# Kernel tuning notes

Hardware: AMD Instinct MI355X
Metric: run time of the kernel (lower is better)

Reference implementation:

```python
import jax, jax.numpy as jnp
import numpy as np

N_SRC = 100000
E = 300000
D = 256
HEADS = 8
D_K = D // HEADS
N_EXPERTS = 5


def setup_inputs() -> dict:
    key = jax.random.key(0)
    kx, ki, ke, kw, kb = jax.random.split(key, 5)
    x = jax.random.normal(kx, (N_SRC, D), dtype=jnp.float32)
    index = jax.random.randint(ki, (E,), 0, N_SRC)
    # disjoint routing masks: each output row handled by exactly one of 5 linears
    expert_id = jax.random.randint(ke, (E,), 0, N_EXPERTS)
    masks = expert_id[None, :] == jnp.arange(N_EXPERTS)[:, None]  # [5, E] bool
    # learned params: 5 independent Linear(D, D) layers (torch layout: y = x @ W.T + b)
    bound = 1.0 / np.sqrt(D)
    W = jax.random.uniform(kw, (N_EXPERTS, D, D), minval=-bound, maxval=bound, dtype=jnp.float32)
    b = jax.random.uniform(kb, (N_EXPERTS, D), minval=-bound, maxval=bound, dtype=jnp.float32)
    return {"x": x, "W": W, "b": b, "index": index, "masks": masks}


def reference(x, W, b, index, masks):
    # gather source rows for every output slot: [E, D]
    xi = x[index]
    out = jnp.zeros((xi.shape[0], D), dtype=x.dtype)
    # sequential masked overwrite matches torch's output[mask] = ... semantics
    for i in range(N_EXPERTS):
        yi = xi @ W[i].T + b[i]  # [E, D]
        out = jnp.where(masks[i][:, None], yi, out)
    return out.reshape(xi.shape[0], HEADS, D_K)
```

## Files before the change

kernel.cpp:

```cpp
#include <hip/hip_runtime.h>

#define E_TOT   300000
#define D_DIM   256
#define N_EXP   5
#define BM      64
#define LDK     264
#define LDF     260
#define NB_CNT  ((E_TOT + 255) / 256)
#define MAX_TILES (E_TOT / BM + N_EXP)

typedef __attribute__((ext_vector_type(8))) short bf16x8;
typedef __attribute__((ext_vector_type(4))) float f32x4;

__device__ inline unsigned short f2bf(float f) {
  union { float f; unsigned u; } v; v.f = f;
  unsigned u = v.u;
  u += 0x7FFFu + ((u >> 16) & 1u);
  return (unsigned short)(u >> 16);
}

__device__ inline int get_expert(const void* masks, int e, bool is_u8) {
  if (is_u8) {
    const unsigned char* m = (const unsigned char*)masks;
#pragma unroll
    for (int i = 0; i < N_EXP; ++i) if (m[(size_t)i * E_TOT + e]) return i;
  } else {
    const int* m = (const int*)masks;
#pragma unroll
    for (int i = 0; i < N_EXP; ++i) if (m[(size_t)i * E_TOT + e]) return i;
  }
  return 0;
}

__global__ void scatter_conv_kernel(const float* __restrict__ W,
                                    unsigned short* __restrict__ Wbf,
                                    const void* __restrict__ masks,
                                    int* __restrict__ cursor, int* __restrict__ perm,
                                    int doConv) {
  __shared__ int wc[4][N_EXP];
  __shared__ int wo[4][N_EXP];
  __shared__ int bb[N_EXP];
  __shared__ int s_u8ok;
  const int tt = threadIdx.x, w = tt >> 6, lane = tt & 63;
  const int e = (int)blockIdx.x * 256 + tt;

  const unsigned char* m8 = (const unsigned char*)masks;
  int cnt1 = 1, ex = -1;
  if (e < E_TOT) {
    cnt1 = 0; int exu = 0;
#pragma unroll
    for (int i = 0; i < N_EXP; ++i) {
      int tb = (m8[(size_t)i * E_TOT + e] != 0);
      cnt1 += tb; if (tb) exu = i;
    }
    ex = exu;
  }
  if (tt == 0) s_u8ok = 1;
  __syncthreads();
  if (cnt1 != 1) s_u8ok = 0;
  __syncthreads();
  if (!s_u8ok && e < E_TOT) ex = get_expert(masks, e, false);

  unsigned long long myBal = 0;
#pragma unroll
  for (int i = 0; i < N_EXP; ++i) {
    unsigned long long bal = __ballot(ex == i);
    if (lane == 0) wc[w][i] = __popcll(bal);
    if (ex == i) myBal = bal;
  }
  if (doConv) {
    const int n4 = (N_EXP * D_DIM * D_DIM) / 4;
    for (int i = e; i < n4; i += (int)gridDim.x * 256) {
      float4 v = ((const float4*)W)[i];
      ushort4 o4;
      o4.x = f2bf(v.x); o4.y = f2bf(v.y); o4.z = f2bf(v.z); o4.w = f2bf(v.w);
      ((ushort4*)Wbf)[i] = o4;
    }
  }
  __syncthreads();
  if (tt < 4 * N_EXP) {
    int ww = tt / N_EXP, ii = tt % N_EXP;
    int s = 0;
    for (int p = 0; p < ww; ++p) s += wc[p][ii];
    wo[ww][ii] = s;
  }
  if (tt < N_EXP) {
    int tot = wc[0][tt] + wc[1][tt] + wc[2][tt] + wc[3][tt];
    int old = atomicAdd(&cursor[tt], tot);
    bb[tt] = tt * E_TOT + old;
  }
  __syncthreads();
  if (ex >= 0) {
    int rank = __popcll(myBal & ((1ull << lane) - 1ull));
    perm[bb[ex] + wo[w][ex] + rank] = e;
  }
}

__global__ void prep_kernel(const float* __restrict__ W, unsigned short* __restrict__ Wbf,
                            const void* __restrict__ masks, int* __restrict__ hdr,
                            int doConv) {
  __shared__ int wc[4][N_EXP];
  __shared__ int s_u8ok;
  const int tt = threadIdx.x, w = tt >> 6, lane = tt & 63;
  const int gtid = (int)blockIdx.x * 256 + tt;

  const unsigned char* m8 = (const unsigned char*)masks;
  int cnt1 = 1, ex = -1;
  if (gtid < E_TOT) {
    cnt1 = 0; int exu = 0;
#pragma unroll
    for (int i = 0; i < N_EXP; ++i) {
      int tb = (m8[(size_t)i * E_TOT + gtid] != 0);
      cnt1 += tb; if (tb) exu = i;
    }
    ex = exu;
  }
  if (tt == 0) s_u8ok = 1;
  __syncthreads();
  if (cnt1 != 1) s_u8ok = 0;
  __syncthreads();
  const int is_u8 = s_u8ok;
  if (!is_u8 && gtid < E_TOT) ex = get_expert(masks, gtid, false);

#pragma unroll
  for (int i = 0; i < N_EXP; ++i) {
    unsigned long long bal = __ballot(ex == i);
    if (lane == 0) wc[w][i] = __popcll(bal);
  }
  if (doConv) {
    const int n4 = (N_EXP * D_DIM * D_DIM) / 4;
    for (int i = gtid; i < n4; i += (int)gridDim.x * 256) {
      float4 v = ((const float4*)W)[i];
      ushort4 o4;
      o4.x = f2bf(v.x); o4.y = f2bf(v.y); o4.z = f2bf(v.z); o4.w = f2bf(v.w);
      ((ushort4*)Wbf)[i] = o4;
    }
  }
  __syncthreads();
  if (tt < N_EXP)
    atomicAdd(&hdr[tt], wc[0][tt] + wc[1][tt] + wc[2][tt] + wc[3][tt]);
  if (tt == 0 && blockIdx.x == 0) hdr[6] = is_u8;
}

__global__ void scatter_kernel(const void* __restrict__ masks, const int* __restrict__ hdr,
                               int* __restrict__ cursor, int* __restrict__ perm) {
  __shared__ int wc[4][N_EXP];
  __shared__ int wo[4][N_EXP];
  __shared__ int bb[N_EXP];
  const int tt = threadIdx.x, w = tt >> 6, lane = tt & 63;
  const int e = (int)blockIdx.x * 256 + tt;
  const bool is_u8 = (hdr[6] != 0);

  int ex = (e < E_TOT) ? get_expert(masks, e, is_u8) : -1;
  unsigned long long myBal = 0;
#pragma unroll
  for (int i = 0; i < N_EXP; ++i) {
    unsigned long long bal = __ballot(ex == i);
    if (lane == 0) wc[w][i] = __popcll(bal);
    if (ex == i) myBal = bal;
  }
  __syncthreads();
  if (tt < 4 * N_EXP) {
    int ww = tt / N_EXP, ii = tt % N_EXP;
    int s = 0;
    for (int p = 0; p < ww; ++p) s += wc[p][ii];
    wo[ww][ii] = s;
  }
  if (tt < N_EXP) {
    int tot = wc[0][tt] + wc[1][tt] + wc[2][tt] + wc[3][tt];
    int old = atomicAdd(&cursor[tt], tot);
    int base = 0;
    for (int i = 0; i < tt; ++i) base += hdr[i];
    bb[tt] = base + old;
  }
  __syncthreads();
  if (ex >= 0) {
    int rank = __popcll(myBal & ((1ull << lane) - 1ull));
    perm[bb[ex] + wo[w][ex] + rank] = e;
  }
}

template <bool PRE, bool FIXB>
__launch_bounds__(256, 4)
__global__ void gemm_kernel(const float* __restrict__ x, const float* __restrict__ W,
                            const unsigned short* __restrict__ Wbf,
                            const float* __restrict__ bias, const int* __restrict__ index,
                            const int* __restrict__ cnts, const int* __restrict__ perm,
                            float* __restrict__ out) {
  __shared__ __align__(16) unsigned short lA[BM * LDK];
  __shared__ int srcRow[BM];
  __shared__ int outRow[BM];

  int t = (int)blockIdx.x;
  int ex = -1, trow = 0, cnt = 0, accT = 0, base = 0, run = 0;
#pragma unroll
  for (int i = 0; i < N_EXP; ++i) {
    int c = cnts[i];
    int nt = (c + BM - 1) / BM;
    if (ex < 0 && t < accT + nt) { ex = i; trow = t - accT; cnt = c; base = run; }
    accT += nt;
    run += c;
  }
  if (ex < 0) return;
  int row0 = (FIXB ? ex * E_TOT : base) + trow * BM;
  int rows = min(BM, cnt - trow * BM);

  const int tt = threadIdx.x;
  if (tt < BM) {
    int rr = min(tt, rows - 1);
    int e = perm[row0 + rr];
    outRow[tt] = e;
    srcRow[tt] = index[e];
  }
  __syncthreads();

#pragma unroll
  for (int i = 0; i < 16; ++i) {
    int lin = i * 256 + tt;
    int rr = lin >> 6;
    int c4 = lin & 63;
    const float4 v = ((const float4*)(x + (size_t)srcRow[rr] * D_DIM))[c4];
    ushort4 o4;
    o4.x = f2bf(v.x); o4.y = f2bf(v.y); o4.z = f2bf(v.z); o4.w = f2bf(v.w);
    *(ushort4*)&lA[rr * LDK + c4 * 4] = o4;
  }
  __syncthreads();

  const int w = tt >> 6, lane = tt & 63, quad = lane >> 4, l16 = lane & 15;

  f32x4 acc[4][4];
#pragma unroll
  for (int mt = 0; mt < 4; ++mt)
#pragma unroll
    for (int nt = 0; nt < 4; ++nt) acc[mt][nt] = (f32x4){0.f, 0.f, 0.f, 0.f};

#pragma unroll
  for (int ks = 0; ks < 8; ++ks) {
    int k0 = ks * 32 + quad * 8;
    bf16x8 a[4], b[4];
#pragma unroll
    for (int mt = 0; mt < 4; ++mt)
      a[mt] = *(const bf16x8*)&lA[(mt * 16 + l16) * LDK + k0];
#pragma unroll
    for (int nt = 0; nt < 4; ++nt) {
      int col = w * 64 + nt * 16 + l16;
      if (PRE) {
        b[nt] = *(const bf16x8*)&Wbf[((size_t)ex * D_DIM + col) * D_DIM + k0];
      } else {
        const float* wp = W + ((size_t)ex * D_DIM + col) * D_DIM + k0;
        float4 v0 = ((const float4*)wp)[0];
        float4 v1 = ((const float4*)wp)[1];
        bf16x8 bb;
        bb[0] = (short)f2bf(v0.x); bb[1] = (short)f2bf(v0.y);
        bb[2] = (short)f2bf(v0.z); bb[3] = (short)f2bf(v0.w);
        bb[4] = (short)f2bf(v1.x); bb[5] = (short)f2bf(v1.y);
        bb[6] = (short)f2bf(v1.z); bb[7] = (short)f2bf(v1.w);
        b[nt] = bb;
      }
    }
#pragma unroll
    for (int mt = 0; mt < 4; ++mt)
#pragma unroll
      for (int nt = 0; nt < 4; ++nt)
        acc[mt][nt] = __builtin_amdgcn_mfma_f32_16x16x32_bf16(a[mt], b[nt], acc[mt][nt], 0, 0, 0);
  }

  float bv[4];
#pragma unroll
  for (int nt = 0; nt < 4; ++nt) bv[nt] = bias[ex * D_DIM + w * 64 + nt * 16 + l16];

  float* lsf = (float*)lA;
#pragma unroll
  for (int chunk = 0; chunk < 2; ++chunk) {
    __syncthreads();
#pragma unroll
    for (int mtl = 0; mtl < 2; ++mtl) {
      int mt = chunk * 2 + mtl;
#pragma unroll
      for (int nt = 0; nt < 4; ++nt) {
        int col = w * 64 + nt * 16 + l16;
#pragma unroll
        for (int r = 0; r < 4; ++r) {
          int lr = mtl * 16 + quad * 4 + r;
          lsf[lr * LDF + col] = acc[mt][nt][r] + bv[nt];
        }
      }
    }
    __syncthreads();
    int r8 = tt >> 3, c8 = tt & 7;
    int grow = chunk * 32 + r8;
    if (grow < rows) {
      float* op = out + (size_t)outRow[grow] * D_DIM;
#pragma unroll
      for (int j = 0; j < 8; ++j) {
        int c4 = c8 + j * 8;
        f32x4 v4 = *(const f32x4*)&lsf[r8 * LDF + c4 * 4];
        __builtin_nontemporal_store(v4, (f32x4*)(op + c4 * 4));
      }
    }
  }
}

extern "C" void kernel_launch(void* const* d_in, const int* in_sizes, int n_in,
                              void* d_out, int out_size, void* d_ws, size_t ws_size,
                              hipStream_t stream) {
  const float* x     = (const float*)d_in[0];
  const float* W     = (const float*)d_in[1];
  const float* bias  = (const float*)d_in[2];
  const int*   index = (const int*)d_in[3];
  const void*  masks = d_in[4];
  float* out = (float*)d_out;

  int* hdr = (int*)d_ws;
  const size_t wbfB  = (size_t)N_EXP * D_DIM * D_DIM * 2;
  const size_t permB = (size_t)E_TOT * 4;
  const bool fix3 = (ws_size >= 1024 + wbfB + (size_t)N_EXP * permB);
  const bool pre  = fix3 || (ws_size >= 1024 + wbfB + permB);
  size_t off = 1024;
  unsigned short* Wbf = nullptr;
  if (pre) { Wbf = (unsigned short*)((char*)d_ws + off); off += wbfB; }
  int* perm = (int*)((char*)d_ws + off);

  (void)hipMemsetAsync(d_ws, 0, 1024, stream);

  if (fix3) {
    scatter_conv_kernel<<<NB_CNT, 256, 0, stream>>>(W, Wbf, masks, hdr + 16, perm, 1);
    gemm_kernel<true, true><<<MAX_TILES, 256, 0, stream>>>(x, W, Wbf, bias, index,
                                                           hdr + 16, perm, out);
  } else {
    prep_kernel<<<NB_CNT, 256, 0, stream>>>(W, Wbf, masks, hdr, pre ? 1 : 0);
    scatter_kernel<<<NB_CNT, 256, 0, stream>>>(masks, hdr, hdr + 16, perm);
    if (pre)
      gemm_kernel<true, false><<<MAX_TILES, 256, 0, stream>>>(x, W, Wbf, bias, index,
                                                              hdr, perm, out);
    else
      gemm_kernel<false, false><<<MAX_TILES, 256, 0, stream>>>(x, W, Wbf, bias, index,
                                                               hdr, perm, out);
  }
}
```

Baseline: 463.4 us.

## Pre-convert x to bf16 and gather rows into LDS with swizzled direct loads

Adds a bf16 copy of x, converted inside the scatter/conversion kernel when the workspace is large enough. The GEMM then gathers A rows with global_load_lds straight into an XOR-swizzled LDS layout instead of loading fp32, converting in registers and storing to padded LDS. The aim is to halve the bytes moved by the random row gather and to remove the per-tile conversion work. In exchange, every call pays a full read of x and a write of its bf16 copy, and the epilogue now stages 16 rows at a time, which adds block barriers.

```diff
diff --git a/kernel.cpp b/kernel.cpp
--- a/kernel.cpp
+++ b/kernel.cpp
@@ -34,15 +34,18 @@
 
 __global__ void scatter_conv_kernel(const float* __restrict__ W,
                                     unsigned short* __restrict__ Wbf,
+                                    const float* __restrict__ x,
+                                    unsigned short* __restrict__ xbf, int nx4,
                                     const void* __restrict__ masks,
                                     int* __restrict__ cursor, int* __restrict__ perm,
-                                    int doConv) {
+                                    int doConv, int doXconv) {
   __shared__ int wc[4][N_EXP];
   __shared__ int wo[4][N_EXP];
   __shared__ int bb[N_EXP];
   __shared__ int s_u8ok;
   const int tt = threadIdx.x, w = tt >> 6, lane = tt & 63;
   const int e = (int)blockIdx.x * 256 + tt;
+  const int gsz = (int)gridDim.x * 256;
 
   const unsigned char* m8 = (const unsigned char*)masks;
   int cnt1 = 1, ex = -1;
@@ -70,11 +73,19 @@
   }
   if (doConv) {
     const int n4 = (N_EXP * D_DIM * D_DIM) / 4;
-    for (int i = e; i < n4; i += (int)gridDim.x * 256) {
+    for (int i = e; i < n4; i += gsz) {
       float4 v = ((const float4*)W)[i];
       ushort4 o4;
       o4.x = f2bf(v.x); o4.y = f2bf(v.y); o4.z = f2bf(v.z); o4.w = f2bf(v.w);
       ((ushort4*)Wbf)[i] = o4;
+    }
+  }
+  if (doXconv) {
+    for (int i = e; i < nx4; i += gsz) {
+      float4 v = ((const float4*)x)[i];
+      ushort4 o4;
+      o4.x = f2bf(v.x); o4.y = f2bf(v.y); o4.z = f2bf(v.z); o4.w = f2bf(v.w);
+      ((ushort4*)xbf)[i] = o4;
     }
   }
   __syncthreads();
@@ -96,94 +107,11 @@
   }
 }
 
-__global__ void prep_kernel(const float* __restrict__ W, unsigned short* __restrict__ Wbf,
-                            const void* __restrict__ masks, int* __restrict__ hdr,
-                            int doConv) {
-  __shared__ int wc[4][N_EXP];
-  __shared__ int s_u8ok;
-  const int tt = threadIdx.x, w = tt >> 6, lane = tt & 63;
-  const int gtid = (int)blockIdx.x * 256 + tt;
-
-  const unsigned char* m8 = (const unsigned char*)masks;
-  int cnt1 = 1, ex = -1;
-  if (gtid < E_TOT) {
-    cnt1 = 0; int exu = 0;
-#pragma unroll
-    for (int i = 0; i < N_EXP; ++i) {
-      int tb = (m8[(size_t)i * E_TOT + gtid] != 0);
-      cnt1 += tb; if (tb) exu = i;
-    }
-    ex = exu;
-  }
-  if (tt == 0) s_u8ok = 1;
-  __syncthreads();
-  if (cnt1 != 1) s_u8ok = 0;
-  __syncthreads();
-  const int is_u8 = s_u8ok;
-  if (!is_u8 && gtid < E_TOT) ex = get_expert(masks, gtid, false);
-
-#pragma unroll
-  for (int i = 0; i < N_EXP; ++i) {
-    unsigned long long bal = __ballot(ex == i);
-    if (lane == 0) wc[w][i] = __popcll(bal);
-  }
-  if (doConv) {
-    const int n4 = (N_EXP * D_DIM * D_DIM) / 4;
-    for (int i = gtid; i < n4; i += (int)gridDim.x * 256) {
-      float4 v = ((const float4*)W)[i];
-      ushort4 o4;
-      o4.x = f2bf(v.x); o4.y = f2bf(v.y); o4.z = f2bf(v.z); o4.w = f2bf(v.w);
-      ((ushort4*)Wbf)[i] = o4;
-    }
-  }
-  __syncthreads();
-  if (tt < N_EXP)
-    atomicAdd(&hdr[tt], wc[0][tt] + wc[1][tt] + wc[2][tt] + wc[3][tt]);
-  if (tt == 0 && blockIdx.x == 0) hdr[6] = is_u8;
-}
-
-__global__ void scatter_kernel(const void* __restrict__ masks, const int* __restrict__ hdr,
-                               int* __restrict__ cursor, int* __restrict__ perm) {
-  __shared__ int wc[4][N_EXP];
-  __shared__ int wo[4][N_EXP];
-  __shared__ int bb[N_EXP];
-  const int tt = threadIdx.x, w = tt >> 6, lane = tt & 63;
-  const int e = (int)blockIdx.x * 256 + tt;
-  const bool is_u8 = (hdr[6] != 0);
-
-  int ex = (e < E_TOT) ? get_expert(masks, e, is_u8) : -1;
-  unsigned long long myBal = 0;
-#pragma unroll
-  for (int i = 0; i < N_EXP; ++i) {
-    unsigned long long bal = __ballot(ex == i);
-    if (lane == 0) wc[w][i] = __popcll(bal);
-    if (ex == i) myBal = bal;
-  }
-  __syncthreads();
-  if (tt < 4 * N_EXP) {
-    int ww = tt / N_EXP, ii = tt % N_EXP;
-    int s = 0;
-    for (int p = 0; p < ww; ++p) s += wc[p][ii];
-    wo[ww][ii] = s;
-  }
-  if (tt < N_EXP) {
-    int tot = wc[0][tt] + wc[1][tt] + wc[2][tt] + wc[3][tt];
-    int old = atomicAdd(&cursor[tt], tot);
-    int base = 0;
-    for (int i = 0; i < tt; ++i) base += hdr[i];
-    bb[tt] = base + old;
-  }
-  __syncthreads();
-  if (ex >= 0) {
-    int rank = __popcll(myBal & ((1ull << lane) - 1ull));
-    perm[bb[ex] + wo[w][ex] + rank] = e;
-  }
-}
-
-template <bool PRE, bool FIXB>
+template <bool PRE, bool FIXB, bool XPRE>
 __launch_bounds__(256, 4)
 __global__ void gemm_kernel(const float* __restrict__ x, const float* __restrict__ W,
                             const unsigned short* __restrict__ Wbf,
+                            const unsigned short* __restrict__ xbf,
                             const float* __restrict__ bias, const int* __restrict__ index,
                             const int* __restrict__ cnts, const int* __restrict__ perm,
                             float* __restrict__ out) {
@@ -206,6 +134,8 @@
   int rows = min(BM, cnt - trow * BM);
 
   const int tt = threadIdx.x;
+  const int w = tt >> 6, lane = tt & 63, quad = lane >> 4, l16 = lane & 15;
+
   if (tt < BM) {
     int rr = min(tt, rows - 1);
     int e = perm[row0 + rr];
@@ -214,19 +144,32 @@
   }
   __syncthreads();
 
-#pragma unroll
-  for (int i = 0; i < 16; ++i) {
-    int lin = i * 256 + tt;
-    int rr = lin >> 6;
-    int c4 = lin & 63;
-    const float4 v = ((const float4*)(x + (size_t)srcRow[rr] * D_DIM))[c4];
-    ushort4 o4;
-    o4.x = f2bf(v.x); o4.y = f2bf(v.y); o4.z = f2bf(v.z); o4.w = f2bf(v.w);
-    *(ushort4*)&lA[rr * LDK + c4 * 4] = o4;
-  }
-  __syncthreads();
-
-  const int w = tt >> 6, lane = tt & 63, quad = lane >> 4, l16 = lane & 15;
+  if (XPRE) {
+    char* lab = (char*)lA;
+#pragma unroll
+    for (int i = 0; i < 8; ++i) {
+      int r0 = (w << 4) + i * 2;
+      int r = r0 + (lane >> 5);
+      int q = ((lane & 31) * 16) ^ ((r & 7) << 4);
+      const char* gp = (const char*)(xbf + (size_t)srcRow[r] * D_DIM) + q;
+      __builtin_amdgcn_global_load_lds(
+          (const __attribute__((address_space(1))) void*)gp,
+          (__attribute__((address_space(3))) void*)(lab + r0 * 512),
+          16, 0, 0);
+    }
+  } else {
+#pragma unroll
+    for (int i = 0; i < 16; ++i) {
+      int lin = i * 256 + tt;
+      int rr = lin >> 6;
+      int c4 = lin & 63;
+      const float4 v = ((const float4*)(x + (size_t)srcRow[rr] * D_DIM))[c4];
+      ushort4 o4;
+      o4.x = f2bf(v.x); o4.y = f2bf(v.y); o4.z = f2bf(v.z); o4.w = f2bf(v.w);
+      *(ushort4*)&lA[rr * LDK + c4 * 4] = o4;
+    }
+  }
+  __syncthreads();
 
   f32x4 acc[4][4];
 #pragma unroll
@@ -234,13 +177,19 @@
 #pragma unroll
     for (int nt = 0; nt < 4; ++nt) acc[mt][nt] = (f32x4){0.f, 0.f, 0.f, 0.f};
 
+  const char* labr = (const char*)lA;
 #pragma unroll
   for (int ks = 0; ks < 8; ++ks) {
     int k0 = ks * 32 + quad * 8;
     bf16x8 a[4], b[4];
 #pragma unroll
-    for (int mt = 0; mt < 4; ++mt)
-      a[mt] = *(const bf16x8*)&lA[(mt * 16 + l16) * LDK + k0];
+    for (int mt = 0; mt < 4; ++mt) {
+      int r = mt * 16 + l16;
+      if (XPRE)
+        a[mt] = *(const bf16x8*)(labr + r * 512 + ((k0 * 2) ^ ((l16 & 7) << 4)));
+      else
+        a[mt] = *(const bf16x8*)&lA[r * LDK + k0];
+    }
 #pragma unroll
     for (int nt = 0; nt < 4; ++nt) {
       int col = w * 64 + nt * 16 + l16;
@@ -271,33 +220,113 @@
 
   float* lsf = (float*)lA;
 #pragma unroll
-  for (int chunk = 0; chunk < 2; ++chunk) {
+  for (int mt = 0; mt < 4; ++mt) {
     __syncthreads();
 #pragma unroll
-    for (int mtl = 0; mtl < 2; ++mtl) {
-      int mt = chunk * 2 + mtl;
-#pragma unroll
-      for (int nt = 0; nt < 4; ++nt) {
-        int col = w * 64 + nt * 16 + l16;
-#pragma unroll
-        for (int r = 0; r < 4; ++r) {
-          int lr = mtl * 16 + quad * 4 + r;
-          lsf[lr * LDF + col] = acc[mt][nt][r] + bv[nt];
-        }
+    for (int nt = 0; nt < 4; ++nt) {
+      int col = w * 64 + nt * 16 + l16;
+#pragma unroll
+      for (int r = 0; r < 4; ++r) {
+        int lr = quad * 4 + r;
+        lsf[lr * LDF + col] = acc[mt][nt][r] + bv[nt];
       }
     }
     __syncthreads();
-    int r8 = tt >> 3, c8 = tt & 7;
-    int grow = chunk * 32 + r8;
+    int r16 = tt >> 4, c16 = tt & 15;
+    int grow = mt * 16 + r16;
     if (grow < rows) {
       float* op = out + (size_t)outRow[grow] * D_DIM;
 #pragma unroll
-      for (int j = 0; j < 8; ++j) {
-        int c4 = c8 + j * 8;
-        f32x4 v4 = *(const f32x4*)&lsf[r8 * LDF + c4 * 4];
+      for (int j = 0; j < 4; ++j) {
+        int c4 = c16 + j * 16;
+        f32x4 v4 = *(const f32x4*)&lsf[r16 * LDF + c4 * 4];
         __builtin_nontemporal_store(v4, (f32x4*)(op + c4 * 4));
       }
     }
+  }
+}
+
+__global__ void prep_kernel(const float* __restrict__ W, unsigned short* __restrict__ Wbf,
+                            const void* __restrict__ masks, int* __restrict__ hdr,
+                            int doConv) {
+  __shared__ int wc[4][N_EXP];
+  __shared__ int s_u8ok;
+  const int tt = threadIdx.x, w = tt >> 6, lane = tt & 63;
+  const int gtid = (int)blockIdx.x * 256 + tt;
+
+  const unsigned char* m8 = (const unsigned char*)masks;
+  int cnt1 = 1, ex = -1;
+  if (gtid < E_TOT) {
+    cnt1 = 0; int exu = 0;
+#pragma unroll
+    for (int i = 0; i < N_EXP; ++i) {
+      int tb = (m8[(size_t)i * E_TOT + gtid] != 0);
+      cnt1 += tb; if (tb) exu = i;
+    }
+    ex = exu;
+  }
+  if (tt == 0) s_u8ok = 1;
+  __syncthreads();
+  if (cnt1 != 1) s_u8ok = 0;
+  __syncthreads();
+  const int is_u8 = s_u8ok;
+  if (!is_u8 && gtid < E_TOT) ex = get_expert(masks, gtid, false);
+
+#pragma unroll
+  for (int i = 0; i < N_EXP; ++i) {
+    unsigned long long bal = __ballot(ex == i);
+    if (lane == 0) wc[w][i] = __popcll(bal);
+  }
+  if (doConv) {
+    const int n4 = (N_EXP * D_DIM * D_DIM) / 4;
+    for (int i = gtid; i < n4; i += (int)gridDim.x * 256) {
+      float4 v = ((const float4*)W)[i];
+      ushort4 o4;
+      o4.x = f2bf(v.x); o4.y = f2bf(v.y); o4.z = f2bf(v.z); o4.w = f2bf(v.w);
+      ((ushort4*)Wbf)[i] = o4;
+    }
+  }
+  __syncthreads();
+  if (tt < N_EXP)
+    atomicAdd(&hdr[tt], wc[0][tt] + wc[1][tt] + wc[2][tt] + wc[3][tt]);
+  if (tt == 0 && blockIdx.x == 0) hdr[6] = is_u8;
+}
+
+__global__ void scatter_kernel(const void* __restrict__ masks, const int* __restrict__ hdr,
+                               int* __restrict__ cursor, int* __restrict__ perm) {
+  __shared__ int wc[4][N_EXP];
+  __shared__ int wo[4][N_EXP];
+  __shared__ int bb[N_EXP];
+  const int tt = threadIdx.x, w = tt >> 6, lane = tt & 63;
+  const int e = (int)blockIdx.x * 256 + tt;
+  const bool is_u8 = (hdr[6] != 0);
+
+  int ex = (e < E_TOT) ? get_expert(masks, e, is_u8) : -1;
+  unsigned long long myBal = 0;
+#pragma unroll
+  for (int i = 0; i < N_EXP; ++i) {
+    unsigned long long bal = __ballot(ex == i);
+    if (lane == 0) wc[w][i] = __popcll(bal);
+    if (ex == i) myBal = bal;
+  }
+  __syncthreads();
+  if (tt < 4 * N_EXP) {
+    int ww = tt / N_EXP, ii = tt % N_EXP;
+    int s = 0;
+    for (int p = 0; p < ww; ++p) s += wc[p][ii];
+    wo[ww][ii] = s;
+  }
+  if (tt < N_EXP) {
+    int tot = wc[0][tt] + wc[1][tt] + wc[2][tt] + wc[3][tt];
+    int old = atomicAdd(&cursor[tt], tot);
+    int base = 0;
+    for (int i = 0; i < tt; ++i) base += hdr[i];
+    bb[tt] = base + old;
+  }
+  __syncthreads();
+  if (ex >= 0) {
+    int rank = __popcll(myBal & ((1ull << lane) - 1ull));
+    perm[bb[ex] + wo[w][ex] + rank] = e;
   }
 }
 
@@ -314,27 +343,37 @@
   int* hdr = (int*)d_ws;
   const size_t wbfB  = (size_t)N_EXP * D_DIM * D_DIM * 2;
   const size_t permB = (size_t)E_TOT * 4;
-  const bool fix3 = (ws_size >= 1024 + wbfB + (size_t)N_EXP * permB);
+  const size_t xbfB  = (size_t)in_sizes[0] * 2;
+  const int    nx4   = in_sizes[0] / 4;
+
+  const bool xpre = (ws_size >= 1024 + wbfB + (size_t)N_EXP * permB + xbfB);
+  const bool fix3 = xpre || (ws_size >= 1024 + wbfB + (size_t)N_EXP * permB);
   const bool pre  = fix3 || (ws_size >= 1024 + wbfB + permB);
   size_t off = 1024;
   unsigned short* Wbf = nullptr;
   if (pre) { Wbf = (unsigned short*)((char*)d_ws + off); off += wbfB; }
-  int* perm = (int*)((char*)d_ws + off);
+  int* perm = (int*)((char*)d_ws + off); off += (fix3 ? (size_t)N_EXP * permB : permB);
+  unsigned short* xbf = (unsigned short*)((char*)d_ws + off);
 
   (void)hipMemsetAsync(d_ws, 0, 1024, stream);
 
   if (fix3) {
-    scatter_conv_kernel<<<NB_CNT, 256, 0, stream>>>(W, Wbf, masks, hdr + 16, perm, 1);
-    gemm_kernel<true, true><<<MAX_TILES, 256, 0, stream>>>(x, W, Wbf, bias, index,
-                                                           hdr + 16, perm, out);
+    scatter_conv_kernel<<<NB_CNT, 256, 0, stream>>>(W, Wbf, x, xbf, nx4, masks,
+                                                    hdr + 16, perm, 1, xpre ? 1 : 0);
+    if (xpre)
+      gemm_kernel<true, true, true><<<MAX_TILES, 256, 0, stream>>>(
+          x, W, Wbf, xbf, bias, index, hdr + 16, perm, out);
+    else
+      gemm_kernel<true, true, false><<<MAX_TILES, 256, 0, stream>>>(
+          x, W, Wbf, xbf, bias, index, hdr + 16, perm, out);
   } else {
     prep_kernel<<<NB_CNT, 256, 0, stream>>>(W, Wbf, masks, hdr, pre ? 1 : 0);
     scatter_kernel<<<NB_CNT, 256, 0, stream>>>(masks, hdr, hdr + 16, perm);
     if (pre)
-      gemm_kernel<true, false><<<MAX_TILES, 256, 0, stream>>>(x, W, Wbf, bias, index,
-                                                              hdr, perm, out);
+      gemm_kernel<true, false, false><<<MAX_TILES, 256, 0, stream>>>(
+          x, W, Wbf, xbf, bias, index, hdr, perm, out);
     else
-      gemm_kernel<false, false><<<MAX_TILES, 256, 0, stream>>>(x, W, Wbf, bias, index,
-                                                               hdr, perm, out);
-  }
-}
+      gemm_kernel<false, false, false><<<MAX_TILES, 256, 0, stream>>>(
+          x, W, Wbf, xbf, bias, index, hdr, perm, out);
+  }
+}
```

New measurement: 450.2 us. -2.8%, faster.
